# Kernel optimization log

Measured on AMD Instinct MI355X. Metric: run time of the kernel, lower is better.

## Reference

```python
import jax, jax.numpy as jnp
import numpy as np

V, D, H, B, T = 50000, 256, 512, 64, 512
FORGET_BIAS = 1.0  # TF LSTMCell default

def setup_inputs() -> dict:
    key = jax.random.key(0)
    k1, k2, k3, k4 = jax.random.split(key, 4)
    word_indices = jax.random.randint(k1, (B, T), 0, V, dtype=jnp.int32)
    num_words = jax.random.randint(k2, (B,), 1, T + 1, dtype=jnp.int32)
    # Embedding: uniform(-1, 1) per original
    W_emb = jax.random.uniform(k3, (V, D), minval=-1.0, maxval=1.0, dtype=jnp.float32)
    # TF LSTMCell: single kernel [(D+H), 4H] with gate order i, j, f, o; zero bias
    kernel = jax.random.normal(k4, (D + H, 4 * H), dtype=jnp.float32) * 0.02
    bias = jnp.zeros((4 * H,), dtype=jnp.float32)
    return {"word_indices": word_indices, "num_words": num_words,
            "W_emb": W_emb, "kernel": kernel, "bias": bias}

def reference(word_indices, num_words, W_emb, kernel, bias):
    # embedding lookup: [B, T, D]
    x = W_emb[word_indices]
    xs = jnp.swapaxes(x, 0, 1)  # [T, B, D] time-major
    ts = jnp.arange(xs.shape[0])
    c0 = jnp.zeros((word_indices.shape[0], H), dtype=x.dtype)
    h0 = jnp.zeros_like(c0)

    def step(carry, inp):
        c, h = carry
        x_t, t = inp
        gates = jnp.concatenate([x_t, h], axis=-1) @ kernel + bias  # [B, 4H]
        i, j, f, o = jnp.split(gates, 4, axis=-1)
        c_new = jax.nn.sigmoid(f + FORGET_BIAS) * c + jax.nn.sigmoid(i) * jnp.tanh(j)
        h_new = jax.nn.sigmoid(o) * jnp.tanh(c_new)
        # static_rnn sequence_length semantics: copy state through past the end
        mask = (t < num_words)[:, None]
        c = jnp.where(mask, c_new, c)
        h = jnp.where(mask, h_new, h)
        return (c, h), None

    (c_fin, h_fin), _ = jax.lax.scan(step, (c0, h0), (xs, ts))
    # TF LSTM final_state = LSTMStateTuple(c, h); stack for a single array output
    return jnp.stack([c_fin, h_fin], axis=0)  # [2, B, H]
```

## Files before the change

kernel.cpp:

```cpp
#include <hip/hip_runtime.h>
#include <stdint.h>


#define NWG     64
#define NTHR    256
#define TSTEPS  512
#define BATCH   64
#define EDIM    256
#define HID     512
#define GCOLS   2048

typedef __attribute__((ext_vector_type(8))) short short8;
typedef __attribute__((ext_vector_type(4))) float f32x4;


__device__ __forceinline__ unsigned short f2bf(float f) {
  unsigned u = __float_as_uint(f);
  unsigned r = (u + 0x7FFFu + ((u >> 16) & 1u)) >> 16;
  return (unsigned short)r;
}
__device__ __forceinline__ float sigf(float x) {
  x = fminf(fmaxf(x, -30.0f), 30.0f);
  return 1.0f / (1.0f + __expf(-x));
}
__device__ __forceinline__ float tanh_fast(float x) {
  x = fminf(fmaxf(x, -15.0f), 15.0f);
  float e = __expf(-2.0f * x);
  return (1.0f - e) / (1.0f + e);
}

__global__ void init_ws(unsigned* ws, int nwords) {
  int i = blockIdx.x * 256 + threadIdx.x;
  if (i < nwords) ws[i] = 0u;
}

__global__ void embed_k(const int* __restrict__ widx, const float* __restrict__ Wemb,
                        unsigned short* __restrict__ xb) {
  int tb = blockIdx.x;
  int t = tb >> 6, b = tb & 63;
  int wi = widx[b * TSTEPS + t];
  const float* src = Wemb + (size_t)wi * EDIM + threadIdx.x * 4;
  float4 v = *(const float4*)src;
  ushort4 o;
  o.x = f2bf(v.x); o.y = f2bf(v.y); o.z = f2bf(v.z); o.w = f2bf(v.w);
  *(ushort4*)(xb + (size_t)tb * EDIM + threadIdx.x * 4) = o;
}

__device__ __forceinline__ void cell_update(const float* g, const float* bl, int u,
                                            int t, int nw, float& c, float& h) {
  float gi = g[u]      + bl[u];
  float gj = g[8 + u]  + bl[8 + u];
  float gf = g[16 + u] + bl[16 + u];
  float go = g[24 + u] + bl[24 + u];
  float cn = sigf(gf + 1.0f) * c + sigf(gi) * tanh_fast(gj);
  float hn = sigf(go) * tanh_fast(cn);
  if (t < nw) { c = cn; h = hn; }
}

__launch_bounds__(NTHR, 1)
__global__ void lstm_persist(const int* __restrict__ num_words,
                             const int* __restrict__ widx,
                             const float* __restrict__ Wemb,
                             const float* __restrict__ Wk,
                             const float* __restrict__ bias,
                             const unsigned short* __restrict__ xb,
                             unsigned short* __restrict__ hb0,
                             unsigned short* __restrict__ hb1,
                             unsigned* flags,
                             float* __restrict__ out,
                             int has_xb)
{
  __shared__ alignas(16) short Wlds[24576];
  __shared__ float gsc[2304];
  __shared__ float blds[32];
  __shared__ alignas(16) unsigned short hst[512];

  const int tid = threadIdx.x;
  const int u0  = blockIdx.x * 8;

  for (int q = tid; q < 3072; q += NTHR) {
    int lq = q & 63;
    int kkn = q >> 6;
    int nt = (kkn >= 24) ? 1 : 0;
    int kk = kkn - nt * 24;
    int kbase = kk * 32 + ((lq >> 4) << 3);
    int n = (nt << 4) + (lq & 15);
    int gcol = ((n >> 3) << 9) + u0 + (n & 7);
    short8 v;
#pragma unroll
    for (int j = 0; j < 8; ++j)
      v[j] = (short)f2bf(Wk[(size_t)(kbase + j) * GCOLS + gcol]);
    *(short8*)&Wlds[q * 8] = v;
  }
  if (tid < 32) blds[tid] = bias[((tid >> 3) << 9) + u0 + (tid & 7)];

  const int wv   = tid >> 6;
  const int lane = tid & 63;
  const int bb   = wv * 16 + (lane & 15);
  const int kq   = (lane >> 4) << 3;

  const int b1 = tid >> 3, u1 = tid & 7;
  const int b2 = b1 + 32,  u2 = u1;
  const int nw1 = num_words[b1], nw2 = num_words[b2];
  float c1 = 0.f, h1 = 0.f, c2 = 0.f, h2 = 0.f;

  __syncthreads();

  unsigned short* hb[2] = {hb0, hb1};

  for (int t = 0; t < TSTEPS; ++t) {
    f32x4 acc0 = {0.f, 0.f, 0.f, 0.f};
    f32x4 acc1 = {0.f, 0.f, 0.f, 0.f};

    if (has_xb) {
      const unsigned short* xrow = xb + ((size_t)t * BATCH + bb) * EDIM + kq;
#pragma unroll
      for (int kk = 0; kk < 8; ++kk) {
        short8 a  = __builtin_bit_cast(short8, *(const uint4*)(xrow + kk * 32));
        short8 w0 = *(const short8*)&Wlds[((kk)      * 64 + lane) * 8];
        short8 w1 = *(const short8*)&Wlds[((24 + kk) * 64 + lane) * 8];
        acc0 = __builtin_amdgcn_mfma_f32_16x16x32_bf16(a, w0, acc0, 0, 0, 0);
        acc1 = __builtin_amdgcn_mfma_f32_16x16x32_bf16(a, w1, acc1, 0, 0, 0);
      }
    } else {
      int wi = widx[bb * TSTEPS + t];
      const float* erow = Wemb + (size_t)wi * EDIM + kq;
#pragma unroll
      for (int kk = 0; kk < 8; ++kk) {
        float4 f0 = *(const float4*)(erow + kk * 32);
        float4 f1 = *(const float4*)(erow + kk * 32 + 4);
        short8 a;
        a[0] = (short)f2bf(f0.x); a[1] = (short)f2bf(f0.y);
        a[2] = (short)f2bf(f0.z); a[3] = (short)f2bf(f0.w);
        a[4] = (short)f2bf(f1.x); a[5] = (short)f2bf(f1.y);
        a[6] = (short)f2bf(f1.z); a[7] = (short)f2bf(f1.w);
        short8 w0 = *(const short8*)&Wlds[((kk)      * 64 + lane) * 8];
        short8 w1 = *(const short8*)&Wlds[((24 + kk) * 64 + lane) * 8];
        acc0 = __builtin_amdgcn_mfma_f32_16x16x32_bf16(a, w0, acc0, 0, 0, 0);
        acc1 = __builtin_amdgcn_mfma_f32_16x16x32_bf16(a, w1, acc1, 0, 0, 0);
      }
    }

    if (t > 0) {
      if (tid < 64) {
        const unsigned* fp = flags + (tid << 5);
        const unsigned tgt = (unsigned)t;
        for (;;) {
          unsigned v;
          asm volatile("global_load_dword %0, %1, off sc0 sc1\n\t"
                       "s_waitcnt vmcnt(0)"
                       : "=v"(v) : "v"(fp));
          if (__ballot(v >= tgt) == 0xFFFFFFFFFFFFFFFFull) break;
        }
      }
      __syncthreads();
    }

    {
      const unsigned short* hrow = hb[t & 1] + bb * HID + kq;
      uint4 af[16];
#pragma unroll
      for (int kk = 0; kk < 16; ++kk)
        asm volatile("global_load_dwordx4 %0, %1, off sc0 sc1"
                     : "=v"(af[kk]) : "v"(hrow + kk * 32));
      asm volatile("s_waitcnt vmcnt(0)" ::: "memory");
#pragma unroll
      for (int kk = 0; kk < 16; ++kk) {
        short8 a  = __builtin_bit_cast(short8, af[kk]);
        short8 w0 = *(const short8*)&Wlds[((8 + kk)  * 64 + lane) * 8];
        short8 w1 = *(const short8*)&Wlds[((32 + kk) * 64 + lane) * 8];
        acc0 = __builtin_amdgcn_mfma_f32_16x16x32_bf16(a, w0, acc0, 0, 0, 0);
        acc1 = __builtin_amdgcn_mfma_f32_16x16x32_bf16(a, w1, acc1, 0, 0, 0);
      }
    }

#pragma unroll
    for (int r = 0; r < 4; ++r) {
      int row = ((lane >> 4) << 2) + r;
      gsc[wv * 576 + row * 36 + (lane & 15)]      = acc0[r];
      gsc[wv * 576 + row * 36 + 16 + (lane & 15)] = acc1[r];
    }
    __syncthreads();

    {
      const float* g = &gsc[((b1 >> 4) * 576) + ((b1 & 15) * 36)];
      cell_update(g, blds, u1, t, nw1, c1, h1);
      hst[(b1 << 3) + u1] = f2bf(h1);
    }
    {
      const float* g = &gsc[((b2 >> 4) * 576) + ((b2 & 15) * 36)];
      cell_update(g, blds, u2, t, nw2, c2, h2);
      hst[(b2 << 3) + u2] = f2bf(h2);
    }

    if (t + 1 < TSTEPS) {
      unsigned short* hw = hb[(t + 1) & 1];
      __syncthreads();
      {
        int bs = tid >> 2, p = tid & 3;
        unsigned v = *(const unsigned*)&hst[(bs << 3) + (p << 1)];
        unsigned* dst = (unsigned*)(hw + (size_t)bs * HID + u0) + p;
        asm volatile("global_store_dword %0, %1, off sc0 sc1"
                     :: "v"(dst), "v"(v) : "memory");
      }
      asm volatile("s_waitcnt vmcnt(0)" ::: "memory");
      __syncthreads();
      if (tid == 0) {
        unsigned* fa = flags + ((unsigned)blockIdx.x << 5);
        unsigned fv = (unsigned)(t + 1);
        asm volatile("global_store_dword %0, %1, off sc0 sc1"
                     :: "v"(fa), "v"(fv) : "memory");
      }
    }
  }

  out[b1 * HID + u0 + u1]         = c1;
  out[32768 + b1 * HID + u0 + u1] = h1;
  out[b2 * HID + u0 + u2]         = c2;
  out[32768 + b2 * HID + u0 + u2] = h2;
}

extern "C" void kernel_launch(void* const* d_in, const int* in_sizes, int n_in,
                              void* d_out, int out_size, void* d_ws, size_t ws_size,
                              hipStream_t stream) {
  const int*   widx = (const int*)d_in[0];
  const int*   nw   = (const int*)d_in[1];
  const float* Wemb = (const float*)d_in[2];
  const float* Wk   = (const float*)d_in[3];
  const float* bias = (const float*)d_in[4];
  float* out = (float*)d_out;
  char* ws = (char*)d_ws;

  unsigned* flags = (unsigned*)(ws + 256);
  unsigned short* hb0 = (unsigned short*)(ws + 8448);
  unsigned short* hb1 = (unsigned short*)(ws + 73984);
  unsigned short* xb  = (unsigned short*)(ws + 139520);

  size_t need = 139520ull + (size_t)TSTEPS * BATCH * EDIM * 2;
  int has_xb = (ws_size >= need) ? 1 : 0;

  size_t init_bytes = ws_size < 139520ull ? ws_size : 139520ull;
  int init_words = (int)(init_bytes / 4);
  init_ws<<<(init_words + 255) / 256, 256, 0, stream>>>((unsigned*)ws, init_words);
  if (has_xb)
    embed_k<<<TSTEPS * BATCH, 64, 0, stream>>>(widx, Wemb, xb);

  void* args[] = {(void*)&nw, (void*)&widx, (void*)&Wemb, (void*)&Wk, (void*)&bias,
                  (void*)&xb, (void*)&hb0, (void*)&hb1, (void*)&flags,
                  (void*)&out, (void*)&has_xb};
  hipLaunchCooperativeKernel((void*)lstm_persist, dim3(NWG), dim3(NTHR), args, 0, stream);
}
```

Measured before the change: 2.819 ms.

## Halve persistent workgroups to 32 with 16 hidden units each and prefetch x

Each persistent workgroup now owns 16 hidden units (64 gate columns) instead of 8, so 32 workgroups cover the hidden state. This halves the number of blocks taking part in the per-step cross-workgroup flag barrier, at the cost of doubling the MFMA work and LDS weight footprint per block. The input-embedding operands for the next step are prefetched into registers during the current step. The cell update is vectorized to four units per thread with packed 64-bit h stores, which drops the extra LDS staging buffer and one __syncthreads per step. The added per-block compute lengthens the serial critical path of each timestep.

```diff
diff --git a/kernel.cpp b/kernel.cpp
--- a/kernel.cpp
+++ b/kernel.cpp
@@ -2,7 +2,7 @@
 #include <stdint.h>
 
 
-#define NWG     64
+#define NWG     32
 #define NTHR    256
 #define TSTEPS  512
 #define BATCH   64
@@ -44,17 +44,6 @@
   ushort4 o;
   o.x = f2bf(v.x); o.y = f2bf(v.y); o.z = f2bf(v.z); o.w = f2bf(v.w);
   *(ushort4*)(xb + (size_t)tb * EDIM + threadIdx.x * 4) = o;
-}
-
-__device__ __forceinline__ void cell_update(const float* g, const float* bl, int u,
-                                            int t, int nw, float& c, float& h) {
-  float gi = g[u]      + bl[u];
-  float gj = g[8 + u]  + bl[8 + u];
-  float gf = g[16 + u] + bl[16 + u];
-  float go = g[24 + u] + bl[24 + u];
-  float cn = sigf(gf + 1.0f) * c + sigf(gi) * tanh_fast(gj);
-  float hn = sigf(go) * tanh_fast(cn);
-  if (t < nw) { c = cn; h = hn; }
 }
 
 __launch_bounds__(NTHR, 1)
@@ -70,58 +59,76 @@
                              float* __restrict__ out,
                              int has_xb)
 {
-  __shared__ alignas(16) short Wlds[24576];
-  __shared__ float gsc[2304];
-  __shared__ float blds[32];
-  __shared__ alignas(16) unsigned short hst[512];
+  __shared__ alignas(16) short Wlds[49152];
+  __shared__ float gsc[4352];
+  __shared__ float blds[64];
 
   const int tid = threadIdx.x;
-  const int u0  = blockIdx.x * 8;
-
-  for (int q = tid; q < 3072; q += NTHR) {
-    int lq = q & 63;
-    int kkn = q >> 6;
-    int nt = (kkn >= 24) ? 1 : 0;
-    int kk = kkn - nt * 24;
+  const int u0  = blockIdx.x * 16;
+
+  for (int q = tid; q < 6144; q += NTHR) {
+    int g   = q / 1536;
+    int rem = q - g * 1536;
+    int kk  = rem >> 6;
+    int lq  = rem & 63;
     int kbase = kk * 32 + ((lq >> 4) << 3);
-    int n = (nt << 4) + (lq & 15);
-    int gcol = ((n >> 3) << 9) + u0 + (n & 7);
+    int gcol  = (g << 9) + u0 + (lq & 15);
     short8 v;
 #pragma unroll
     for (int j = 0; j < 8; ++j)
       v[j] = (short)f2bf(Wk[(size_t)(kbase + j) * GCOLS + gcol]);
     *(short8*)&Wlds[q * 8] = v;
   }
-  if (tid < 32) blds[tid] = bias[((tid >> 3) << 9) + u0 + (tid & 7)];
+  if (tid < 64) blds[tid] = bias[((tid >> 4) << 9) + u0 + (tid & 15)];
 
   const int wv   = tid >> 6;
   const int lane = tid & 63;
   const int bb   = wv * 16 + (lane & 15);
   const int kq   = (lane >> 4) << 3;
 
-  const int b1 = tid >> 3, u1 = tid & 7;
-  const int b2 = b1 + 32,  u2 = u1;
-  const int nw1 = num_words[b1], nw2 = num_words[b2];
-  float c1 = 0.f, h1 = 0.f, c2 = 0.f, h2 = 0.f;
+  const int eb = tid >> 2, uq = tid & 3;
+  const int nwb = num_words[eb];
+  float cst[4] = {0.f, 0.f, 0.f, 0.f};
+  float hsv[4] = {0.f, 0.f, 0.f, 0.f};
 
   __syncthreads();
 
+  const float bI[4] = {blds[uq*4+0], blds[uq*4+1], blds[uq*4+2], blds[uq*4+3]};
+  const float bJ[4] = {blds[16+uq*4+0], blds[16+uq*4+1], blds[16+uq*4+2], blds[16+uq*4+3]};
+  const float bF[4] = {blds[32+uq*4+0], blds[32+uq*4+1], blds[32+uq*4+2], blds[32+uq*4+3]};
+  const float bO[4] = {blds[48+uq*4+0], blds[48+uq*4+1], blds[48+uq*4+2], blds[48+uq*4+3]};
+
   unsigned short* hb[2] = {hb0, hb1};
 
+  uint4 xf[8];
+  if (has_xb) {
+    const unsigned short* xr = xb + (size_t)bb * EDIM + kq;
+#pragma unroll
+    for (int kk = 0; kk < 8; ++kk)
+      asm volatile("global_load_dwordx4 %0, %1, off" : "=v"(xf[kk]) : "v"(xr + kk * 32));
+  }
+
   for (int t = 0; t < TSTEPS; ++t) {
-    f32x4 acc0 = {0.f, 0.f, 0.f, 0.f};
-    f32x4 acc1 = {0.f, 0.f, 0.f, 0.f};
+    f32x4 acc[4];
+    acc[0] = (f32x4){0.f,0.f,0.f,0.f}; acc[1] = (f32x4){0.f,0.f,0.f,0.f};
+    acc[2] = (f32x4){0.f,0.f,0.f,0.f}; acc[3] = (f32x4){0.f,0.f,0.f,0.f};
 
     if (has_xb) {
-      const unsigned short* xrow = xb + ((size_t)t * BATCH + bb) * EDIM + kq;
+      asm volatile("s_waitcnt vmcnt(0)" ::: "memory");
 #pragma unroll
       for (int kk = 0; kk < 8; ++kk) {
-        short8 a  = __builtin_bit_cast(short8, *(const uint4*)(xrow + kk * 32));
-        short8 w0 = *(const short8*)&Wlds[((kk)      * 64 + lane) * 8];
-        short8 w1 = *(const short8*)&Wlds[((24 + kk) * 64 + lane) * 8];
-        acc0 = __builtin_amdgcn_mfma_f32_16x16x32_bf16(a, w0, acc0, 0, 0, 0);
-        acc1 = __builtin_amdgcn_mfma_f32_16x16x32_bf16(a, w1, acc1, 0, 0, 0);
-      }
+        short8 a = __builtin_bit_cast(short8, xf[kk]);
+#pragma unroll
+        for (int g = 0; g < 4; ++g) {
+          short8 w = *(const short8*)&Wlds[((g * 24 + kk) * 64 + lane) * 8];
+          acc[g] = __builtin_amdgcn_mfma_f32_16x16x32_bf16(a, w, acc[g], 0, 0, 0);
+        }
+      }
+      int tn = (t + 1 < TSTEPS) ? t + 1 : t;
+      const unsigned short* xr = xb + ((size_t)tn * BATCH + bb) * EDIM + kq;
+#pragma unroll
+      for (int kk = 0; kk < 8; ++kk)
+        asm volatile("global_load_dwordx4 %0, %1, off" : "=v"(xf[kk]) : "v"(xr + kk * 32));
     } else {
       int wi = widx[bb * TSTEPS + t];
       const float* erow = Wemb + (size_t)wi * EDIM + kq;
@@ -134,24 +141,24 @@
         a[2] = (short)f2bf(f0.z); a[3] = (short)f2bf(f0.w);
         a[4] = (short)f2bf(f1.x); a[5] = (short)f2bf(f1.y);
         a[6] = (short)f2bf(f1.z); a[7] = (short)f2bf(f1.w);
-        short8 w0 = *(const short8*)&Wlds[((kk)      * 64 + lane) * 8];
-        short8 w1 = *(const short8*)&Wlds[((24 + kk) * 64 + lane) * 8];
-        acc0 = __builtin_amdgcn_mfma_f32_16x16x32_bf16(a, w0, acc0, 0, 0, 0);
-        acc1 = __builtin_amdgcn_mfma_f32_16x16x32_bf16(a, w1, acc1, 0, 0, 0);
+#pragma unroll
+        for (int g = 0; g < 4; ++g) {
+          short8 w = *(const short8*)&Wlds[((g * 24 + kk) * 64 + lane) * 8];
+          acc[g] = __builtin_amdgcn_mfma_f32_16x16x32_bf16(a, w, acc[g], 0, 0, 0);
+        }
       }
     }
 
     if (t > 0) {
-      if (tid < 64) {
+      if (tid < NWG) {
         const unsigned* fp = flags + (tid << 5);
         const unsigned tgt = (unsigned)t;
-        for (;;) {
-          unsigned v;
+        unsigned v;
+        do {
           asm volatile("global_load_dword %0, %1, off sc0 sc1\n\t"
                        "s_waitcnt vmcnt(0)"
                        : "=v"(v) : "v"(fp));
-          if (__ballot(v >= tgt) == 0xFFFFFFFFFFFFFFFFull) break;
-        }
+        } while (v < tgt);
       }
       __syncthreads();
     }
@@ -163,46 +170,58 @@
       for (int kk = 0; kk < 16; ++kk)
         asm volatile("global_load_dwordx4 %0, %1, off sc0 sc1"
                      : "=v"(af[kk]) : "v"(hrow + kk * 32));
+      asm volatile("s_waitcnt vmcnt(8)" ::: "memory");
       asm volatile("s_waitcnt vmcnt(0)" ::: "memory");
 #pragma unroll
       for (int kk = 0; kk < 16; ++kk) {
-        short8 a  = __builtin_bit_cast(short8, af[kk]);
-        short8 w0 = *(const short8*)&Wlds[((8 + kk)  * 64 + lane) * 8];
-        short8 w1 = *(const short8*)&Wlds[((32 + kk) * 64 + lane) * 8];
-        acc0 = __builtin_amdgcn_mfma_f32_16x16x32_bf16(a, w0, acc0, 0, 0, 0);
-        acc1 = __builtin_amdgcn_mfma_f32_16x16x32_bf16(a, w1, acc1, 0, 0, 0);
+        short8 a = __builtin_bit_cast(short8, af[kk]);
+#pragma unroll
+        for (int g = 0; g < 4; ++g) {
+          short8 w = *(const short8*)&Wlds[((g * 24 + 8 + kk) * 64 + lane) * 8];
+          acc[g] = __builtin_amdgcn_mfma_f32_16x16x32_bf16(a, w, acc[g], 0, 0, 0);
+        }
       }
     }
 
 #pragma unroll
     for (int r = 0; r < 4; ++r) {
       int row = ((lane >> 4) << 2) + r;
-      gsc[wv * 576 + row * 36 + (lane & 15)]      = acc0[r];
-      gsc[wv * 576 + row * 36 + 16 + (lane & 15)] = acc1[r];
+      float* dst = &gsc[wv * 1088 + row * 68 + (lane & 15)];
+      dst[0]  = acc[0][r];
+      dst[16] = acc[1][r];
+      dst[32] = acc[2][r];
+      dst[48] = acc[3][r];
     }
     __syncthreads();
 
     {
-      const float* g = &gsc[((b1 >> 4) * 576) + ((b1 & 15) * 36)];
-      cell_update(g, blds, u1, t, nw1, c1, h1);
-      hst[(b1 << 3) + u1] = f2bf(h1);
-    }
-    {
-      const float* g = &gsc[((b2 >> 4) * 576) + ((b2 & 15) * 36)];
-      cell_update(g, blds, u2, t, nw2, c2, h2);
-      hst[(b2 << 3) + u2] = f2bf(h2);
+      const float* g0 = &gsc[(eb >> 4) * 1088 + (eb & 15) * 68 + uq * 4];
+      float4 gI = *(const float4*)(g0);
+      float4 gJ = *(const float4*)(g0 + 16);
+      float4 gF = *(const float4*)(g0 + 32);
+      float4 gO = *(const float4*)(g0 + 48);
+      float gi[4] = {gI.x, gI.y, gI.z, gI.w};
+      float gj[4] = {gJ.x, gJ.y, gJ.z, gJ.w};
+      float gf[4] = {gF.x, gF.y, gF.z, gF.w};
+      float go[4] = {gO.x, gO.y, gO.z, gO.w};
+      bool live = (t < nwb);
+#pragma unroll
+      for (int m = 0; m < 4; ++m) {
+        float cn = sigf(gf[m] + bF[m] + 1.0f) * cst[m] +
+                   sigf(gi[m] + bI[m]) * tanh_fast(gj[m] + bJ[m]);
+        float hn = sigf(go[m] + bO[m]) * tanh_fast(cn);
+        if (live) { cst[m] = cn; hsv[m] = hn; }
+      }
     }
 
     if (t + 1 < TSTEPS) {
       unsigned short* hw = hb[(t + 1) & 1];
-      __syncthreads();
-      {
-        int bs = tid >> 2, p = tid & 3;
-        unsigned v = *(const unsigned*)&hst[(bs << 3) + (p << 1)];
-        unsigned* dst = (unsigned*)(hw + (size_t)bs * HID + u0) + p;
-        asm volatile("global_store_dword %0, %1, off sc0 sc1"
-                     :: "v"(dst), "v"(v) : "memory");
-      }
+      unsigned lo = (unsigned)f2bf(hsv[0]) | ((unsigned)f2bf(hsv[1]) << 16);
+      unsigned hi = (unsigned)f2bf(hsv[2]) | ((unsigned)f2bf(hsv[3]) << 16);
+      unsigned long long pv = (unsigned long long)lo | ((unsigned long long)hi << 32);
+      unsigned* dst = (unsigned*)(hw + (size_t)eb * HID + u0 + uq * 4);
+      asm volatile("global_store_dwordx2 %0, %1, off sc0 sc1"
+                   :: "v"(dst), "v"(pv) : "memory");
       asm volatile("s_waitcnt vmcnt(0)" ::: "memory");
       __syncthreads();
       if (tid == 0) {
@@ -214,10 +233,12 @@
     }
   }
 
-  out[b1 * HID + u0 + u1]         = c1;
-  out[32768 + b1 * HID + u0 + u1] = h1;
-  out[b2 * HID + u0 + u2]         = c2;
-  out[32768 + b2 * HID + u0 + u2] = h2;
+  {
+    float* oc = out + eb * HID + u0 + uq * 4;
+    float* oh = out + 32768 + eb * HID + u0 + uq * 4;
+    *(float4*)oc = (float4){cst[0], cst[1], cst[2], cst[3]};
+    *(float4*)oh = (float4){hsv[0], hsv[1], hsv[2], hsv[3]};
+  }
 }
 
 extern "C" void kernel_launch(void* const* d_in, const int* in_sizes, int n_in,
@@ -248,5 +269,5 @@
   void* args[] = {(void*)&nw, (void*)&widx, (void*)&Wemb, (void*)&Wk, (void*)&bias,
                   (void*)&xb, (void*)&hb0, (void*)&hb1, (void*)&flags,
                   (void*)&out, (void*)&has_xb};
-  hipLaunchCooperativeKernel((void*)lstm_persist, dim3(NWG), dim3(NTHR), args, 0, stream);
-}
+  (void)hipLaunchCooperativeKernel((void*)lstm_persist, dim3(NWG), dim3(NTHR), args, 0, stream);
+}
```

New measurement: 3.162 ms. +12.1%, slower.
